# Kernel optimization log

Hardware: AMD Instinct MI355X
Metric: run time of the kernel (lower is better)

Reference implementation:

```python
import jax, jax.numpy as jnp
import numpy as np

NUM_BLK, BLK_LEN, MAX_WORDLEN = 32, 128, 16
CHAR_VOCAB, CHAR_EMB = 262, 16
CONV_FN = (128, 256, 512, 1024)
CONV_FW = (2, 3, 4, 5)
INPUT_DIM = int(sum(CONV_FN))  # 1920
HIDDEN = 256       # hidden_dim == hidden_dimg (required by fc / fc1 shapes)
INPUT_DIMG = 256
VOCAB = 32000

PARAM_NAMES = ["char_embed", "conv_w0", "conv_b0", "conv_w1", "conv_b1", "conv_w2", "conv_b2",
               "conv_w3", "conv_b3", "hw_nonl_w", "hw_nonl_b", "hw_gate_w", "hw_gate_b",
               "lstm_Wih", "lstm_Whh", "lstm_bih", "lstm_bhh", "fc1_w", "fc1_b",
               "g_Wih", "g_Whh", "g_bih", "g_bhh", "fc_w", "fc_b", "fc_out_w", "fc_out_b"]


def _lstm(x, W_ih, W_hh, b_ih, b_hh):
    """PyTorch-convention LSTM. x: [T, B, D] -> outputs [T, B, H]. Zero init state."""
    H = W_hh.shape[1]
    B = x.shape[1]

    def step(carry, xt):
        h, c = carry
        gates = xt @ W_ih.T + b_ih + h @ W_hh.T + b_hh
        i, f, g, o = jnp.split(gates, 4, axis=-1)  # PyTorch gate order i,f,g,o
        c = jax.nn.sigmoid(f) * c + jax.nn.sigmoid(i) * jnp.tanh(g)
        h = jax.nn.sigmoid(o) * jnp.tanh(c)
        return (h, c), h

    h0 = jnp.zeros((B, H), x.dtype)
    _, ys = jax.lax.scan(step, (h0, h0), x)
    return ys


def _forward(inputs, p):
    # char embedding: [num_blk*blk_len, max_wordlen, char_emb]
    emb = p["char_embed"][inputs.reshape(-1, MAX_WORDLEN)]
    feats = []
    for i in range(len(CONV_FN)):
        # 1D conv over word-length axis (conv2d with H=1 in the original)
        y = jax.lax.conv_general_dilated(emb, p[f"conv_w{i}"], (1,), "VALID",
                                         dimension_numbers=("NWC", "WIO", "NWC")) + p[f"conv_b{i}"]
        feats.append(jnp.max(jnp.tanh(y), axis=1))  # max over time -> [N, fn_i]
    cc = jnp.concatenate(feats, axis=-1).reshape(NUM_BLK, BLK_LEN, INPUT_DIM)

    # highway layer
    nonl = jax.nn.relu(cc @ p["hw_nonl_w"].T + p["hw_nonl_b"])
    gate = jax.nn.sigmoid(cc @ p["hw_gate_w"].T + p["hw_gate_b"])
    hw = gate * nonl + (1.0 - gate) * cc

    # local LSTM: seq=blk_len, vectorized across num_blk as batch (zero init state,
    # matching the reused all-zero self.hidden per block)
    out = _lstm(hw.transpose(1, 0, 2), p["lstm_Wih"], p["lstm_Whh"], p["lstm_bih"], p["lstm_bhh"])
    outblks = out.transpose(1, 0, 2)  # [num_blk, blk_len, H]

    # max_pool1d / avg_pool1d with kernel 2 over the feature axis, then concat
    pr = outblks.reshape(NUM_BLK, BLK_LEN, HIDDEN // 2, 2)
    pooled = jnp.concatenate([pr.max(axis=-1), pr.mean(axis=-1)], axis=-1)  # [nb, bl, H]

    blkrep = pooled.reshape(NUM_BLK, BLK_LEN * HIDDEN) @ p["fc1_w"].T + p["fc1_b"]  # [nb, dimg]

    # global LSTM over blocks (batch=1, seq=num_blk)
    out_glb = _lstm(blkrep[:, None, :], p["g_Wih"], p["g_Whh"], p["g_bih"], p["g_bhh"])[:, 0, :]

    # fused replacement of the per-(i,j) loop: block i>0 uses out_glb[i-1];
    # block 0 is left as zeros (the original only assigns outf inside the else branch)
    glob = jnp.broadcast_to(out_glb[:-1, None, :], (NUM_BLK - 1, BLK_LEN, HIDDEN))
    x = jnp.concatenate([outblks[1:], glob], axis=-1)              # [nb-1, bl, 2H]
    fcd = x @ p["fc_w"].T + p["fc_b"]                              # [nb-1, bl, H]
    outf = jnp.concatenate([jnp.zeros((1, BLK_LEN, HIDDEN), fcd.dtype), fcd], axis=0)
    outf = outf @ p["fc_out_w"].T + p["fc_out_b"]                  # [nb, bl, vocab]
    return outf, outblks


def setup_inputs() -> dict:
    key = jax.random.key(0)
    ks = iter(jax.random.split(key, 40))

    def rn(shape, s=0.05):
        return jax.random.normal(next(ks), shape, dtype=jnp.float32) * s

    inp = {}
    inp["inputs"] = jax.random.randint(next(ks), (NUM_BLK, BLK_LEN, MAX_WORDLEN), 0, CHAR_VOCAB, dtype=jnp.int32)
    inp["char_embed"] = rn((CHAR_VOCAB, CHAR_EMB), 0.1).at[1].set(0.0)  # padding_idx=1
    for i, (fn, fw) in enumerate(zip(CONV_FN, CONV_FW)):
        inp[f"conv_w{i}"] = rn((fw, CHAR_EMB, fn))  # WIO layout
        inp[f"conv_b{i}"] = rn((fn,))
    inp["hw_nonl_w"] = rn((INPUT_DIM, INPUT_DIM), 0.02)
    inp["hw_nonl_b"] = rn((INPUT_DIM,))
    inp["hw_gate_w"] = rn((INPUT_DIM, INPUT_DIM), 0.02)
    inp["hw_gate_b"] = jax.random.uniform(next(ks), (INPUT_DIM,), dtype=jnp.float32, minval=-2.05, maxval=2.05)
    inp["lstm_Wih"] = rn((4 * HIDDEN, INPUT_DIM))
    inp["lstm_Whh"] = rn((4 * HIDDEN, HIDDEN))
    inp["lstm_bih"] = rn((4 * HIDDEN,))
    inp["lstm_bhh"] = rn((4 * HIDDEN,))
    inp["fc1_w"] = rn((INPUT_DIMG, HIDDEN * BLK_LEN), 0.01)
    inp["fc1_b"] = rn((INPUT_DIMG,))
    inp["g_Wih"] = rn((4 * HIDDEN, INPUT_DIMG))
    inp["g_Whh"] = rn((4 * HIDDEN, HIDDEN))
    inp["g_bih"] = rn((4 * HIDDEN,))
    inp["g_bhh"] = rn((4 * HIDDEN,))
    inp["fc_w"] = rn((HIDDEN, 2 * HIDDEN))
    inp["fc_b"] = rn((HIDDEN,))
    inp["fc_out_w"] = rn((VOCAB, HIDDEN))
    inp["fc_out_b"] = rn((VOCAB,))
    return inp


def reference(inputs, char_embed, conv_w0, conv_b0, conv_w1, conv_b1, conv_w2, conv_b2,
              conv_w3, conv_b3, hw_nonl_w, hw_nonl_b, hw_gate_w, hw_gate_b,
              lstm_Wih, lstm_Whh, lstm_bih, lstm_bhh, fc1_w, fc1_b,
              g_Wih, g_Whh, g_bih, g_bhh, fc_w, fc_b, fc_out_w, fc_out_b):
    args = locals()
    p = {k: args[k] for k in PARAM_NAMES}
    return _forward(inputs, p)
```

## Files before the change

kernel.cpp:

```cpp
#include <hip/hip_runtime.h>
#include <cstdint>
#include <cstddef>

#define NBLK 32
#define BLEN 128
#define WLEN 16
#define CEMB 16
#define NWRD 4096
#define IDIM 1920
#define HID  256
#define G4   1024
#define VOC  32000

typedef __attribute__((ext_vector_type(8))) short short8;
typedef __attribute__((ext_vector_type(4))) float f32x4;
typedef unsigned short u16;

static __device__ __forceinline__ float sigf(float x){ return 1.f/(1.f+__expf(-x)); }
static __device__ __forceinline__ u16 f2bf(float f){
  unsigned u = __float_as_uint(f);
  u = (u + 0x7fffu + ((u >> 16) & 1u)) >> 16;
  return (u16)u;
}

__global__ __launch_bounds__(256) void k_prep_conv(
    const float* __restrict__ cw0, const float* __restrict__ cb0,
    const float* __restrict__ cw1, const float* __restrict__ cb1,
    const float* __restrict__ cw2, const float* __restrict__ cb2,
    const float* __restrict__ cw3, const float* __restrict__ cb3,
    u16* __restrict__ Wt, float* __restrict__ ball)
{
  int f = blockIdx.x*256 + threadIdx.x;
  if (f >= IDIM) return;
  int fl, fw, fn; const float* W; const float* B;
  if (f < 128)      { fl=f;     fw=2; fn=128;  W=cw0; B=cb0; }
  else if (f < 384) { fl=f-128; fw=3; fn=256;  W=cw1; B=cb1; }
  else if (f < 896) { fl=f-384; fw=4; fn=512;  W=cw2; B=cb2; }
  else              { fl=f-896; fw=5; fn=1024; W=cw3; B=cb3; }
  ball[f] = B[fl];
  int kmax = fw*CEMB;
  for (int k = 0; k < 96; ++k)
    Wt[(size_t)f*96 + k] = (k < kmax) ? f2bf(W[(size_t)k*fn + fl]) : (u16)0;
}

__global__ __launch_bounds__(256) void k_conv_mfma(
    const int* __restrict__ inp, const float* __restrict__ ctab,
    const u16* __restrict__ Wt, const float* __restrict__ ball,
    float* __restrict__ cc, u16* __restrict__ ccbf)
{
  __shared__ __align__(16) u16 E[2][384];
  int tid = threadIdx.x;
  int n0 = blockIdx.x * 2;
  int wv = tid >> 6, l = tid & 63;
  int lr = l & 15, lk = l >> 4;

  for (int idx = tid; idx < 512; idx += 256) {
    int ws_ = idx >> 8, w = (idx >> 4) & 15, c = idx & 15;
    int ch = inp[(n0 + ws_)*WLEN + w];
    E[ws_][w*CEMB + c] = f2bf(ctab[ch*CEMB + c]);
  }
  for (int idx = tid; idx < 256; idx += 256) {
    int ws_ = idx >> 7;
    E[ws_][256 + (idx & 127)] = 0;
  }
  __syncthreads();

  short8 af[2][3];
#pragma unroll
  for (int ks = 0; ks < 3; ++ks) {
    int gk = ks*32 + lk*8;
    int w_ = gk >> 4, c0 = gk & 15;
    af[0][ks] = *(const short8*)&E[0][(lr + w_)*CEMB + c0];
    af[1][ks] = *(const short8*)&E[1][(lr + w_)*CEMB + c0];
  }

  for (int j = 0; j < 30; ++j) {
    int tile = wv*30 + j;
    int L = (tile < 8) ? 15 : (tile < 24 ? 14 : (tile < 56 ? 13 : 12));
    const u16* wp = Wt + (size_t)(tile*16 + lr)*96 + lk*8;
    short8 b0 = *(const short8*)(wp);
    short8 b1 = *(const short8*)(wp + 32);
    short8 b2 = *(const short8*)(wp + 64);
    f32x4 a0 = {}, a1 = {};
    a0 = __builtin_amdgcn_mfma_f32_16x16x32_bf16(af[0][0], b0, a0, 0, 0, 0);
    a1 = __builtin_amdgcn_mfma_f32_16x16x32_bf16(af[1][0], b0, a1, 0, 0, 0);
    a0 = __builtin_amdgcn_mfma_f32_16x16x32_bf16(af[0][1], b1, a0, 0, 0, 0);
    a1 = __builtin_amdgcn_mfma_f32_16x16x32_bf16(af[1][1], b1, a1, 0, 0, 0);
    a0 = __builtin_amdgcn_mfma_f32_16x16x32_bf16(af[0][2], b2, a0, 0, 0, 0);
    a1 = __builtin_amdgcn_mfma_f32_16x16x32_bf16(af[1][2], b2, a1, 0, 0, 0);
    float m0 = -1e30f, m1 = -1e30f;
#pragma unroll
    for (int r = 0; r < 4; ++r) {
      int i = lk*4 + r;
      if (i < L) { m0 = fmaxf(m0, a0[r]); m1 = fmaxf(m1, a1[r]); }
    }
    m0 = fmaxf(m0, __shfl_xor(m0, 16)); m0 = fmaxf(m0, __shfl_xor(m0, 32));
    m1 = fmaxf(m1, __shfl_xor(m1, 16)); m1 = fmaxf(m1, __shfl_xor(m1, 32));
    if (lk == 0) {
      int f = tile*16 + lr;
      float bv = ball[f];
      float v0 = tanhf(m0 + bv), v1 = tanhf(m1 + bv);
      cc[(size_t)n0*IDIM + f]       = v0;
      cc[(size_t)(n0+1)*IDIM + f]   = v1;
      ccbf[(size_t)n0*IDIM + f]     = f2bf(v0);
      ccbf[(size_t)(n0+1)*IDIM + f] = f2bf(v1);
    }
  }
}

__global__ __launch_bounds__(256) void k_highway_mfma(
    const u16* __restrict__ Abf,
    const float* __restrict__ ccf,
    const u16* __restrict__ Wn, const float* __restrict__ bn,
    const u16* __restrict__ Wg, const float* __restrict__ bg,
    u16* __restrict__ outbf)
{
  int tN = blockIdx.x * 64, tM = blockIdx.y * 64;
  int tid = threadIdx.x;
  int wave = tid >> 6, lane = tid & 63;
  int wm = (wave >> 1) * 32, wn = (wave & 1) * 32;
  int lhi = lane >> 4, llo = lane & 15;
  f32x4 aN[2][2] = {}, aG[2][2] = {};
  for (int k0 = 0; k0 < IDIM; k0 += 32) {
    int kof = k0 + lhi*8;
    short8 a0 = *(const short8*)(Abf + (size_t)(tM + wm + llo)*IDIM + kof);
    short8 a1 = *(const short8*)(Abf + (size_t)(tM + wm + 16 + llo)*IDIM + kof);
    short8 n0 = *(const short8*)(Wn + (size_t)(tN + wn + llo)*IDIM + kof);
    short8 n1 = *(const short8*)(Wn + (size_t)(tN + wn + 16 + llo)*IDIM + kof);
    short8 g0 = *(const short8*)(Wg + (size_t)(tN + wn + llo)*IDIM + kof);
    short8 g1 = *(const short8*)(Wg + (size_t)(tN + wn + 16 + llo)*IDIM + kof);
    aN[0][0] = __builtin_amdgcn_mfma_f32_16x16x32_bf16(a0, n0, aN[0][0], 0, 0, 0);
    aN[0][1] = __builtin_amdgcn_mfma_f32_16x16x32_bf16(a0, n1, aN[0][1], 0, 0, 0);
    aN[1][0] = __builtin_amdgcn_mfma_f32_16x16x32_bf16(a1, n0, aN[1][0], 0, 0, 0);
    aN[1][1] = __builtin_amdgcn_mfma_f32_16x16x32_bf16(a1, n1, aN[1][1], 0, 0, 0);
    aG[0][0] = __builtin_amdgcn_mfma_f32_16x16x32_bf16(a0, g0, aG[0][0], 0, 0, 0);
    aG[0][1] = __builtin_amdgcn_mfma_f32_16x16x32_bf16(a0, g1, aG[0][1], 0, 0, 0);
    aG[1][0] = __builtin_amdgcn_mfma_f32_16x16x32_bf16(a1, g0, aG[1][0], 0, 0, 0);
    aG[1][1] = __builtin_amdgcn_mfma_f32_16x16x32_bf16(a1, g1, aG[1][1], 0, 0, 0);
  }
#pragma unroll
  for (int mi = 0; mi < 2; ++mi)
#pragma unroll
    for (int ni = 0; ni < 2; ++ni) {
      int col = tN + wn + ni*16 + llo;
      float bnv = bn[col], bgv = bg[col];
#pragma unroll
      for (int r = 0; r < 4; ++r) {
        int row = tM + wm + mi*16 + lhi*4 + r;
        float nl = fmaxf(aN[mi][ni][r] + bnv, 0.f);
        float gt = sigf(aG[mi][ni][r] + bgv);
        float ccv = ccf[(size_t)row*IDIM + col];
        outbf[(size_t)row*IDIM + col] = f2bf(gt*nl + (1.f-gt)*ccv);
      }
    }
}

__global__ __launch_bounds__(256) void k_gemm_bf16(
    const u16* __restrict__ Abf, const u16* __restrict__ Bbf,
    const float* __restrict__ b1, const float* __restrict__ b2,
    float* __restrict__ C, int M, int N, int K)
{
  int tN = blockIdx.x * 64, tM = blockIdx.y * 64;
  int tid = threadIdx.x;
  int wave = tid >> 6, lane = tid & 63;
  int wm = (wave >> 1) * 32, wn = (wave & 1) * 32;
  int lhi = lane >> 4, llo = lane & 15;
  f32x4 acc[2][2] = {};
  for (int k0 = 0; k0 < K; k0 += 32) {
    int kof = k0 + lhi*8;
    short8 a0 = *(const short8*)(Abf + (size_t)(tM + wm + llo)*K + kof);
    short8 a1 = *(const short8*)(Abf + (size_t)(tM + wm + 16 + llo)*K + kof);
    short8 b0 = *(const short8*)(Bbf + (size_t)(tN + wn + llo)*K + kof);
    short8 b1v = *(const short8*)(Bbf + (size_t)(tN + wn + 16 + llo)*K + kof);
    acc[0][0] = __builtin_amdgcn_mfma_f32_16x16x32_bf16(a0, b0,  acc[0][0], 0, 0, 0);
    acc[0][1] = __builtin_amdgcn_mfma_f32_16x16x32_bf16(a0, b1v, acc[0][1], 0, 0, 0);
    acc[1][0] = __builtin_amdgcn_mfma_f32_16x16x32_bf16(a1, b0,  acc[1][0], 0, 0, 0);
    acc[1][1] = __builtin_amdgcn_mfma_f32_16x16x32_bf16(a1, b1v, acc[1][1], 0, 0, 0);
  }
#pragma unroll
  for (int mi = 0; mi < 2; ++mi)
#pragma unroll
    for (int ni = 0; ni < 2; ++ni) {
      int col = tN + wn + ni*16 + llo;
      float bv = b1[col] + (b2 ? b2[col] : 0.f);
#pragma unroll
      for (int r = 0; r < 4; ++r) {
        int row = tM + wm + mi*16 + lhi*4 + r;
        C[(size_t)row*N + col] = acc[mi][ni][r] + bv;
      }
    }
}

__global__ __launch_bounds__(256) void k_gemm_f32(
    const float* __restrict__ A, const float* __restrict__ B,
    const float* __restrict__ b1, const float* __restrict__ b2,
    float* __restrict__ C, int M, int N, int K)
{
  __shared__ float As[16][68], Bs[16][68];
  int tM = blockIdx.x * 64, tN = blockIdx.y * 64;
  int tid = threadIdx.x, tx = tid & 15, ty = tid >> 4;
  float acc[4][4] = {};
  for (int k0 = 0; k0 < K; k0 += 16) {
    for (int i = tid; i < 1024; i += 256) {
      int m = i >> 4, k = i & 15;
      As[k][m] = A[(size_t)(tM+m)*K + k0 + k];
      Bs[k][m] = B[(size_t)(tN+m)*K + k0 + k];
    }
    __syncthreads();
#pragma unroll
    for (int kk = 0; kk < 16; ++kk) {
      float4 av = *(const float4*)&As[kk][ty*4];
      float4 bv = *(const float4*)&Bs[kk][tx*4];
      float a[4] = {av.x,av.y,av.z,av.w};
      float b[4] = {bv.x,bv.y,bv.z,bv.w};
#pragma unroll
      for (int i = 0; i < 4; ++i)
#pragma unroll
        for (int j = 0; j < 4; ++j) acc[i][j] += a[i]*b[j];
    }
    __syncthreads();
  }
  for (int i = 0; i < 4; ++i) {
    int row = tM + ty*4 + i;
    for (int j = 0; j < 4; ++j) {
      int col = tN + tx*4 + j;
      float v = acc[i][j] + b1[col] + (b2 ? b2[col] : 0.f);
      C[(size_t)row*N + col] = v;
    }
  }
}

__global__ __launch_bounds__(512, 2) void k_lstm_rec(
    const float* __restrict__ xp,
    const u16* __restrict__ whhbf,
    float* __restrict__ out,
    int nsteps)
{
  __shared__ __align__(16) u16 WL[65536];
  __shared__ __align__(16) u16 hS[256];
  __shared__ __align__(16) float gS[1024];
  int tid = threadIdx.x;
  int w = tid >> 6, l = tid & 63;
  int lr = l & 15, lk = l >> 4;

  for (int c = tid; c < 8192; c += 512) {
    int row = c >> 5, slot = c & 31;
    short8 v = *(const short8*)&whhbf[(size_t)(768 + row)*HID + slot*8];
    *(short8*)&WL[row*HID + ((slot ^ (row & 7)) << 3)] = v;
  }

  short8 af[6][8];
#pragma unroll
  for (int t2 = 0; t2 < 6; ++t2)
#pragma unroll
    for (int ks = 0; ks < 8; ++ks)
      af[t2][ks] = *(const short8*)&whhbf[(size_t)(w*96 + t2*16 + lr)*HID + ks*32 + lk*8];

  if (tid < 256) hS[tid] = 0;
  float c_st = 0.f;
  __syncthreads();

  const float* xpb = xp + (size_t)blockIdx.x * nsteps * G4;
  float* outb = out + (size_t)blockIdx.x * nsteps * HID;

  for (int t = 0; t < nsteps; ++t) {
    float xi = 0.f, xf = 0.f, xg = 0.f, xo = 0.f;
    if (tid < 256) {
      const float* xr = xpb + (size_t)t*G4;
      xi = xr[tid]; xf = xr[256+tid]; xg = xr[512+tid]; xo = xr[768+tid];
    }
    f32x4 a[6] = {};
#pragma unroll
    for (int ks = 0; ks < 8; ++ks) {
      short8 bfk = *(const short8*)&hS[ks*32 + lk*8];
#pragma unroll
      for (int t2 = 0; t2 < 6; ++t2)
        a[t2] = __builtin_amdgcn_mfma_f32_16x16x32_bf16(af[t2][ks], bfk, a[t2], 0, 0, 0);
    }
    f32x4 b0 = {}, b1 = {};
    {
      int r0 = w*32 + lr, r1 = r0 + 16;
#pragma unroll
      for (int ks = 0; ks < 8; ++ks) {
        short8 bfk = *(const short8*)&hS[ks*32 + lk*8];
        int slot = ks*4 + lk;
        short8 w0 = *(const short8*)&WL[r0*HID + ((slot ^ (r0 & 7)) << 3)];
        short8 w1 = *(const short8*)&WL[r1*HID + ((slot ^ (r1 & 7)) << 3)];
        b0 = __builtin_amdgcn_mfma_f32_16x16x32_bf16(w0, bfk, b0, 0, 0, 0);
        b1 = __builtin_amdgcn_mfma_f32_16x16x32_bf16(w1, bfk, b1, 0, 0, 0);
      }
    }
    if ((l & 15) == 0) {
#pragma unroll
      for (int t2 = 0; t2 < 6; ++t2)
        *(f32x4*)&gS[w*96 + t2*16 + lk*4] = a[t2];
      *(f32x4*)&gS[768 + w*32 + lk*4]      = b0;
      *(f32x4*)&gS[768 + w*32 + 16 + lk*4] = b1;
    }
    __syncthreads();
    if (tid < 256) {
      float iv = sigf(gS[tid] + xi);
      float fv = sigf(gS[256+tid] + xf);
      float gv = tanhf(gS[512+tid] + xg);
      float ov = sigf(gS[768+tid] + xo);
      c_st = fv*c_st + iv*gv;
      float h = ov*tanhf(c_st);
      hS[tid] = f2bf(h);
      outb[(size_t)t*HID + tid] = h;
    }
    __syncthreads();
  }
}

__global__ __launch_bounds__(256) void k_pool(const float* __restrict__ ob, float* __restrict__ pooled)
{
  int idx = blockIdx.x*256 + threadIdx.x;
  int n = idx >> 7, p = idx & 127;
  float a = ob[(size_t)n*HID + 2*p];
  float b = ob[(size_t)n*HID + 2*p + 1];
  pooled[(size_t)n*HID + p]       = fmaxf(a, b);
  pooled[(size_t)n*HID + 128 + p] = 0.5f*(a + b);
}

__global__ __launch_bounds__(256) void k_fc1(
    const float* __restrict__ pooled, const float* __restrict__ W,
    const float* __restrict__ bias, float* __restrict__ blkrep)
{
  __shared__ float buf[256];
  int b = blockIdx.x, cg = blockIdx.y, tid = threadIdx.x;
  const float* pb = pooled + (size_t)b*32768;
  float s[16] = {};
  for (int k = tid; k < 32768; k += 256) {
    float pv = pb[k];
#pragma unroll
    for (int cl = 0; cl < 16; ++cl)
      s[cl] += pv * W[(size_t)(cg*16 + cl)*32768 + k];
  }
  for (int cl = 0; cl < 16; ++cl) {
    buf[tid] = s[cl];
    __syncthreads();
    for (int off = 128; off; off >>= 1) {
      if (tid < off) buf[tid] += buf[tid + off];
      __syncthreads();
    }
    if (tid == 0) blkrep[b*HID + cg*16 + cl] = buf[0] + bias[cg*16 + cl];
    __syncthreads();
  }
}

__global__ __launch_bounds__(256) void k_gather(
    const float* __restrict__ ob, const float* __restrict__ og, float* __restrict__ A2)
{
  int idx = blockIdx.x*256 + threadIdx.x;
  int r = idx >> 9, jc = idx & 511;
  int i = 1 + (r >> 7), t = r & 127;
  float v = (jc < 256) ? ob[(size_t)(i*BLEN + t)*HID + jc]
                       : og[(i-1)*HID + (jc - 256)];
  A2[idx] = v;
}

__global__ __launch_bounds__(256) void k_make_outfpre(
    const float* __restrict__ fcd, u16* __restrict__ o)
{
  int idx = blockIdx.x*256 + threadIdx.x;
  int row = idx >> 8;
  float v = (row < 128) ? 0.f : fcd[(size_t)(row - 128)*HID + (idx & 255)];
  o[idx] = f2bf(v);
}

__global__ __launch_bounds__(256) void k_cvt_bf16(const float* __restrict__ in, u16* __restrict__ o, int n)
{
  int idx = blockIdx.x*256 + threadIdx.x;
  if (idx < n) o[idx] = f2bf(in[idx]);
}

__global__ __launch_bounds__(256) void k_fcout(
    const u16* __restrict__ Abf,
    const u16* __restrict__ Wbf,
    const float* __restrict__ bias,
    float* __restrict__ out)
{
  __shared__ __align__(16) float T[64][260];
  int tW = blockIdx.x * 64;
  int tV = blockIdx.y * 256;
  int tid = threadIdx.x;
  int wave = tid >> 6, lane = tid & 63;
  int lhi = lane >> 4, llo = lane & 15;
  int vbase = tV + wave*64;

  f32x4 acc[4][4] = {};
  const int K = HID;
  for (int k0 = 0; k0 < K; k0 += 32) {
    int kof = k0 + lhi*8;
    short8 vfrag[4], wfrag[4];
#pragma unroll
    for (int mt = 0; mt < 4; ++mt)
      vfrag[mt] = *(const short8*)(Wbf + (size_t)(vbase + mt*16 + llo)*K + kof);
#pragma unroll
    for (int nt = 0; nt < 4; ++nt)
      wfrag[nt] = *(const short8*)(Abf + (size_t)(tW + nt*16 + llo)*K + kof);
#pragma unroll
    for (int mt = 0; mt < 4; ++mt)
#pragma unroll
      for (int nt = 0; nt < 4; ++nt)
        acc[mt][nt] = __builtin_amdgcn_mfma_f32_16x16x32_bf16(vfrag[mt], wfrag[nt], acc[mt][nt], 0, 0, 0);
  }
#pragma unroll
  for (int nt = 0; nt < 4; ++nt) {
    int wrow = nt*16 + llo;
#pragma unroll
    for (int mt = 0; mt < 4; ++mt)
      *(f32x4*)&T[wrow][wave*64 + mt*16 + lhi*4] = acc[mt][nt];
  }
  __syncthreads();
  f32x4 bv = *(const f32x4*)&bias[tV + lane*4];
#pragma unroll
  for (int i = 0; i < 16; ++i) {
    int wrow = wave*16 + i;
    f32x4 v = *(const f32x4*)&T[wrow][lane*4];
    v += bv;
    __builtin_nontemporal_store(v, (f32x4*)&out[(size_t)(tW + wrow)*VOC + tV + lane*4]);
  }
}

extern "C" void kernel_launch(void* const* d_in, const int* in_sizes, int n_in,
                              void* d_out, int out_size, void* d_ws, size_t ws_size,
                              hipStream_t stream) {
  (void)in_sizes; (void)n_in; (void)out_size; (void)ws_size;
  const int*   inp   = (const int*)d_in[0];
  const float* cemb  = (const float*)d_in[1];
  const float* cw0   = (const float*)d_in[2];
  const float* cb0   = (const float*)d_in[3];
  const float* cw1   = (const float*)d_in[4];
  const float* cb1   = (const float*)d_in[5];
  const float* cw2   = (const float*)d_in[6];
  const float* cb2   = (const float*)d_in[7];
  const float* cw3   = (const float*)d_in[8];
  const float* cb3   = (const float*)d_in[9];
  const float* hwnW  = (const float*)d_in[10];
  const float* hwnB  = (const float*)d_in[11];
  const float* hwgW  = (const float*)d_in[12];
  const float* hwgB  = (const float*)d_in[13];
  const float* lWih  = (const float*)d_in[14];
  const float* lWhh  = (const float*)d_in[15];
  const float* lbih  = (const float*)d_in[16];
  const float* lbhh  = (const float*)d_in[17];
  const float* fc1W  = (const float*)d_in[18];
  const float* fc1B  = (const float*)d_in[19];
  const float* gWih  = (const float*)d_in[20];
  const float* gWhh  = (const float*)d_in[21];
  const float* gbih  = (const float*)d_in[22];
  const float* gbhh  = (const float*)d_in[23];
  const float* fcW   = (const float*)d_in[24];
  const float* fcB   = (const float*)d_in[25];
  const float* foW   = (const float*)d_in[26];
  const float* foB   = (const float*)d_in[27];

  float* ws      = (float*)d_ws;
  float* cc      = ws;
  float* xproj   = cc      + (size_t)NWRD*IDIM;
  float* pooled  = xproj   + (size_t)NWRD*G4;
  float* blkrep  = pooled  + (size_t)NWRD*HID;
  float* out_glb = blkrep  + 64*HID;
  float* A2      = out_glb + NBLK*HID;
  float* fcd     = A2      + (size_t)3968*512;
  float* ball    = fcd     + (size_t)3968*HID;
  u16*   apre    = (u16*)(ball + 2048);
  u16*   wbf     = apre    + (size_t)NWRD*HID;
  u16*   whhLbf  = wbf     + (size_t)VOC*HID;
  u16*   whhGbf  = whhLbf  + (size_t)G4*HID;
  u16*   wtall   = whhGbf  + (size_t)G4*HID;
  u16*   ccbf    = wtall   + 184320 + 64;
  u16*   hwbf    = ccbf    + (size_t)NWRD*IDIM;
  u16*   wnbf    = hwbf    + (size_t)NWRD*IDIM;
  u16*   wgbf    = wnbf    + (size_t)IDIM*IDIM;
  u16*   wihbf   = wgbf    + (size_t)IDIM*IDIM;

  float* outf    = (float*)d_out;
  float* outblks = outf + (size_t)NWRD*VOC;

  k_prep_conv<<<8, 256, 0, stream>>>(cw0, cb0, cw1, cb1, cw2, cb2, cw3, cb3, wtall, ball);
  k_cvt_bf16<<<(IDIM*IDIM)/256, 256, 0, stream>>>(hwnW, wnbf, IDIM*IDIM);
  k_cvt_bf16<<<(IDIM*IDIM)/256, 256, 0, stream>>>(hwgW, wgbf, IDIM*IDIM);
  k_cvt_bf16<<<(G4*IDIM)/256, 256, 0, stream>>>(lWih, wihbf, G4*IDIM);
  k_cvt_bf16<<<(G4*HID)/256, 256, 0, stream>>>(lWhh, whhLbf, G4*HID);
  k_cvt_bf16<<<(G4*HID)/256, 256, 0, stream>>>(gWhh, whhGbf, G4*HID);
  k_cvt_bf16<<<(VOC*HID)/256, 256, 0, stream>>>(foW, wbf, VOC*HID);
  k_conv_mfma<<<NWRD/2, 256, 0, stream>>>(inp, cemb, wtall, ball, cc, ccbf);
  k_highway_mfma<<<dim3(IDIM/64, NWRD/64), 256, 0, stream>>>(ccbf, cc, wnbf, hwnB, wgbf, hwgB, hwbf);
  k_gemm_bf16<<<dim3(G4/64, NWRD/64), 256, 0, stream>>>(hwbf, wihbf, lbih, lbhh, xproj, NWRD, G4, IDIM);
  k_lstm_rec<<<NBLK, 512, 0, stream>>>(xproj, whhLbf, outblks, BLEN);
  k_pool<<<(NWRD*128)/256, 256, 0, stream>>>(outblks, pooled);
  k_fc1<<<dim3(NBLK, 16), 256, 0, stream>>>(pooled, fc1W, fc1B, blkrep);
  k_gemm_f32<<<dim3(1, G4/64), 256, 0, stream>>>(blkrep, gWih, gbih, gbhh, A2, 64, G4, HID);
  k_lstm_rec<<<1, 512, 0, stream>>>(A2, whhGbf, out_glb, NBLK);
  k_gather<<<(3968*512)/256, 256, 0, stream>>>(outblks, out_glb, A2);
  k_gemm_f32<<<dim3(3968/64, HID/64), 256, 0, stream>>>(A2, fcW, fcB, nullptr, fcd, 3968, HID, 512);
  k_make_outfpre<<<(NWRD*HID)/256, 256, 0, stream>>>(fcd, apre);
  k_fcout<<<dim3(NWRD/64, VOC/256), 256, 0, stream>>>(apre, wbf, foB, outf);
}
```

Measured before the change: 1.419 ms.

## Fuse LSTM gate math into MFMA lanes with double-buffered h and x

Reassigns the recurrent weight rows so each wave owns matching i/f/g/o rows for the same hidden units, letting the gate nonlinearities run directly on MFMA accumulators. This removes the gate scratch buffer and one of the two block barriers per timestep. The next step's input projections are prefetched into a double-buffered shared array and h is double-buffered so only one sync per step is needed. Only one lane per 16 computes redundantly across replicated columns, and all lanes do the transcendental work, which adds some redundant ALU work per step.

```diff
diff --git a/kernel.cpp b/kernel.cpp
--- a/kernel.cpp
+++ b/kernel.cpp
@@ -13,6 +13,7 @@
 #define VOC  32000
 
 typedef __attribute__((ext_vector_type(8))) short short8;
+typedef __attribute__((ext_vector_type(4))) short short4s;
 typedef __attribute__((ext_vector_type(4))) float f32x4;
 typedef unsigned short u16;
 
@@ -237,8 +238,8 @@
     int nsteps)
 {
   __shared__ __align__(16) u16 WL[65536];
-  __shared__ __align__(16) u16 hS[256];
-  __shared__ __align__(16) float gS[1024];
+  __shared__ __align__(16) u16 hS[2][256];
+  __shared__ __align__(16) float xS[2][1024];
   int tid = threadIdx.x;
   int w = tid >> 6, l = tid & 63;
   int lr = l & 15, lk = l >> 4;
@@ -251,62 +252,74 @@
 
   short8 af[6][8];
 #pragma unroll
-  for (int t2 = 0; t2 < 6; ++t2)
+  for (int t2 = 0; t2 < 6; ++t2) {
+    int row = (t2 >> 1)*256 + 32*w + 16*(t2 & 1) + lr;
 #pragma unroll
     for (int ks = 0; ks < 8; ++ks)
-      af[t2][ks] = *(const short8*)&whhbf[(size_t)(w*96 + t2*16 + lr)*HID + ks*32 + lk*8];
-
-  if (tid < 256) hS[tid] = 0;
-  float c_st = 0.f;
-  __syncthreads();
+      af[t2][ks] = *(const short8*)&whhbf[(size_t)row*HID + ks*32 + lk*8];
+  }
 
   const float* xpb = xp + (size_t)blockIdx.x * nsteps * G4;
   float* outb = out + (size_t)blockIdx.x * nsteps * HID;
 
+  if (tid < 256) hS[0][tid] = 0;
+  xS[0][tid]       = xpb[tid];
+  xS[0][512 + tid] = xpb[512 + tid];
+  float cst[2][4] = {};
+  __syncthreads();
+
+  int r0 = 32*w + lr, r1 = r0 + 16;
   for (int t = 0; t < nsteps; ++t) {
-    float xi = 0.f, xf = 0.f, xg = 0.f, xo = 0.f;
-    if (tid < 256) {
-      const float* xr = xpb + (size_t)t*G4;
-      xi = xr[tid]; xf = xr[256+tid]; xg = xr[512+tid]; xo = xr[768+tid];
-    }
-    f32x4 a[6] = {};
+    int cur = t & 1, nxt = cur ^ 1;
+    float nx0 = 0.f, nx1 = 0.f;
+    if (t + 1 < nsteps) {
+      const float* xr = xpb + (size_t)(t + 1)*G4;
+      nx0 = xr[tid]; nx1 = xr[512 + tid];
+    }
+    f32x4 acc[8] = {};
 #pragma unroll
     for (int ks = 0; ks < 8; ++ks) {
-      short8 bfk = *(const short8*)&hS[ks*32 + lk*8];
+      short8 bfk = *(const short8*)&hS[cur][ks*32 + lk*8];
 #pragma unroll
       for (int t2 = 0; t2 < 6; ++t2)
-        a[t2] = __builtin_amdgcn_mfma_f32_16x16x32_bf16(af[t2][ks], bfk, a[t2], 0, 0, 0);
-    }
-    f32x4 b0 = {}, b1 = {};
-    {
-      int r0 = w*32 + lr, r1 = r0 + 16;
-#pragma unroll
-      for (int ks = 0; ks < 8; ++ks) {
-        short8 bfk = *(const short8*)&hS[ks*32 + lk*8];
-        int slot = ks*4 + lk;
-        short8 w0 = *(const short8*)&WL[r0*HID + ((slot ^ (r0 & 7)) << 3)];
-        short8 w1 = *(const short8*)&WL[r1*HID + ((slot ^ (r1 & 7)) << 3)];
-        b0 = __builtin_amdgcn_mfma_f32_16x16x32_bf16(w0, bfk, b0, 0, 0, 0);
-        b1 = __builtin_amdgcn_mfma_f32_16x16x32_bf16(w1, bfk, b1, 0, 0, 0);
+        acc[t2] = __builtin_amdgcn_mfma_f32_16x16x32_bf16(af[t2][ks], bfk, acc[t2], 0, 0, 0);
+      int slot = ks*4 + lk;
+      short8 w0 = *(const short8*)&WL[r0*HID + ((slot ^ (r0 & 7)) << 3)];
+      short8 w1 = *(const short8*)&WL[r1*HID + ((slot ^ (r1 & 7)) << 3)];
+      acc[6] = __builtin_amdgcn_mfma_f32_16x16x32_bf16(w0, bfk, acc[6], 0, 0, 0);
+      acc[7] = __builtin_amdgcn_mfma_f32_16x16x32_bf16(w1, bfk, acc[7], 0, 0, 0);
+    }
+    xS[nxt][tid] = nx0; xS[nxt][512 + tid] = nx1;
+    float hf[2][4];
+#pragma unroll
+    for (int sub = 0; sub < 2; ++sub) {
+      int jb = 32*w + 16*sub + lk*4;
+      f32x4 xi = *(const f32x4*)&xS[cur][jb];
+      f32x4 xf = *(const f32x4*)&xS[cur][256 + jb];
+      f32x4 xg = *(const f32x4*)&xS[cur][512 + jb];
+      f32x4 xo = *(const f32x4*)&xS[cur][768 + jb];
+#pragma unroll
+      for (int r = 0; r < 4; ++r) {
+        float iv = sigf(acc[sub][r]     + xi[r]);
+        float fv = sigf(acc[2 + sub][r] + xf[r]);
+        float gv = tanhf(acc[4 + sub][r] + xg[r]);
+        float ov = sigf(acc[6 + sub][r] + xo[r]);
+        float c2 = fv*cst[sub][r] + iv*gv;
+        cst[sub][r] = c2;
+        hf[sub][r] = ov*tanhf(c2);
       }
     }
-    if ((l & 15) == 0) {
-#pragma unroll
-      for (int t2 = 0; t2 < 6; ++t2)
-        *(f32x4*)&gS[w*96 + t2*16 + lk*4] = a[t2];
-      *(f32x4*)&gS[768 + w*32 + lk*4]      = b0;
-      *(f32x4*)&gS[768 + w*32 + 16 + lk*4] = b1;
-    }
-    __syncthreads();
-    if (tid < 256) {
-      float iv = sigf(gS[tid] + xi);
-      float fv = sigf(gS[256+tid] + xf);
-      float gv = tanhf(gS[512+tid] + xg);
-      float ov = sigf(gS[768+tid] + xo);
-      c_st = fv*c_st + iv*gv;
-      float h = ov*tanhf(c_st);
-      hS[tid] = f2bf(h);
-      outb[(size_t)t*HID + tid] = h;
+    if (lr == 0) {
+#pragma unroll
+      for (int sub = 0; sub < 2; ++sub) {
+        int jb = 32*w + 16*sub + lk*4;
+        short4s hb;
+        f32x4 hv;
+#pragma unroll
+        for (int r = 0; r < 4; ++r) { hb[r] = (short)f2bf(hf[sub][r]); hv[r] = hf[sub][r]; }
+        *(short4s*)&hS[nxt][jb] = hb;
+        *(f32x4*)&outb[(size_t)t*HID + jb] = hv;
+      }
     }
     __syncthreads();
   }
```

After: 1.743 ms. +22.9%, slower.
